# Performance work log

Hardware: AMD Instinct MI355X
Metric: run time of the kernel (lower is better)

The kernel has to match this reference:

```python
import jax, jax.numpy as jnp
import numpy as np

N, E, D, L, RBF = 20000, 320000, 128, 3, 64
CUTOFF = 5.0
LN_EPS = 1e-5


def setup_inputs() -> dict:
    key = jax.random.key(0)
    ks = jax.random.split(key, 20)
    s = 0.05
    inp = {
        'z': jax.random.normal(ks[0], (N, 64), jnp.float32),
        'pos': jax.random.normal(ks[1], (N, 3), jnp.float32),
        'edge_index': jax.random.randint(ks[2], (2, E), 0, N),
        'in_w': jax.random.normal(ks[3], (64, D), jnp.float32) * s,
        'in_b': jnp.zeros((D,), jnp.float32),
        'filt_w': jax.random.normal(ks[4], (RBF, 3 * D), jnp.float32) * s,
        'filt_b': jnp.zeros((3 * D,), jnp.float32),
        'inter_w1': jax.random.normal(ks[5], (L, D, D), jnp.float32) * s,
        'inter_b1': jnp.zeros((L, D), jnp.float32),
        'inter_w2': jax.random.normal(ks[6], (L, D, 3 * D), jnp.float32) * s,
        'inter_b2': jnp.zeros((L, 3 * D), jnp.float32),
        'mix_mu_w': jax.random.normal(ks[7], (L, D, 2 * D), jnp.float32) * s,
        'mix_w1': jax.random.normal(ks[8], (L, 2 * D, D), jnp.float32) * s,
        'mix_b1': jnp.zeros((L, D), jnp.float32),
        'mix_w2': jax.random.normal(ks[9], (L, D, 3 * D), jnp.float32) * s,
        'mix_b2': jnp.zeros((L, 3 * D), jnp.float32),
        'mu_proj_w': jnp.zeros((D,), jnp.float32),  # nn.init.constant_(0.0) in source
        'ln_g': jnp.ones((D,), jnp.float32),
        'ln_b': jnp.zeros((D,), jnp.float32),
    }
    return inp


def painn_forward(z, pos, in_w, in_b, filt_w, filt_b, inter_w1, inter_b1,
                  inter_w2, inter_b2, mix_mu_w, mix_w1, mix_b1, mix_w2, mix_b2,
                  mu_proj_w, ln_g, ln_b, edge_index):
    idx_i, idx_j = edge_index[0], edge_index[1]
    # edge geometry
    r_ij = pos[idx_j] - pos[idx_i]                               # [E,3]
    d_ij = jnp.maximum(jnp.linalg.norm(r_ij, axis=1, keepdims=True), 1e-8)  # [E,1]
    dir_ij = r_ij / d_ij                                          # [E,3]
    # gaussian smearing
    offset = jnp.linspace(0.0, CUTOFF, RBF).astype(jnp.float32)
    coeff = -0.5 / (offset[1] - offset[0]) ** 2
    phi = jnp.exp(coeff * (d_ij - offset) ** 2)                   # [E,RBF]
    # cosine cutoff
    xc = jnp.clip(d_ij / CUTOFF, 0.0, 1.0)
    fcut = 0.5 * (jnp.cos(jnp.pi * xc) + 1.0) * (xc < 1.0)        # [E,1]
    filters = (phi @ filt_w + filt_b) * fcut                      # [E,3D]
    filters = jnp.clip(jnp.nan_to_num(filters), -5.0, 5.0)
    Wij = filters[:, None, :]                                     # [E,1,3D]

    q = jax.nn.silu(z @ in_w + in_b)[:, None, :]                  # [N,1,D]
    mu = jnp.zeros((N, 3, D), q.dtype)                            # [N,3,D]

    for l in range(L):
        # interaction (edge gather -> gate -> scatter-add)
        x = jax.nn.silu(q @ inter_w1[l] + inter_b1[l]) @ inter_w2[l] + inter_b2[l]  # [N,1,3D]
        xj = x[idx_j] * Wij                                       # [E,1,3D]
        dq, dmuR, dmumu = jnp.split(xj, 3, axis=-1)               # each [E,1,D]
        muj = mu[idx_j]                                           # [E,3,D]
        q = q + jax.ops.segment_sum(dq, idx_i, num_segments=N)
        dmu = dmuR * dir_ij[:, :, None] + dmumu * muj             # [E,3,D]
        mu = mu + jax.ops.segment_sum(dmu, idx_i, num_segments=N)
        # intra-atomic mixing
        mu_mix = mu @ mix_mu_w[l]                                  # [N,3,2D]
        mu_V, mu_W = jnp.split(mu_mix, 2, axis=-1)                 # [N,3,D]
        mu_Vn = jnp.sqrt(jnp.sum(mu_V ** 2, axis=-2, keepdims=True) + 1e-8)  # [N,1,D]
        ctx = jnp.concatenate([q, mu_Vn], axis=-1)                 # [N,1,2D]
        xm = jax.nn.silu(ctx @ mix_w1[l] + mix_b1[l]) @ mix_w2[l] + mix_b2[l]  # [N,1,3D]
        dq_i, dmu_i, dqmu_i = jnp.split(xm, 3, axis=-1)
        q = q + dq_i + dqmu_i * jnp.sum(mu_V * mu_W, axis=1, keepdims=True)
        mu = mu + dmu_i * mu_W

    node_attr = jnp.clip(jnp.nan_to_num(q[:, 0, :]), -5.0, 5.0)   # [N,D]
    mean = jnp.mean(node_attr, axis=-1, keepdims=True)
    var = jnp.var(node_attr, axis=-1, keepdims=True)
    node_attr = (node_attr - mean) * jax.lax.rsqrt(var + LN_EPS) * ln_g + ln_b
    node_attr = jnp.nan_to_num(jnp.tanh(node_attr))

    mu = jnp.nan_to_num(mu)
    mu_node = jax.ops.segment_sum(mu[idx_j], idx_i, num_segments=N)  # [N,3,D]
    mu_node = jnp.clip(jnp.nan_to_num(mu_node), -5.0, 5.0)
    pos_attr = jnp.clip(jnp.nan_to_num(mu_node @ mu_proj_w), -5.0, 5.0)  # [N,3]
    return node_attr, pos_attr


def reference(z, pos, edge_index, in_w, in_b, filt_w, filt_b, inter_w1, inter_b1,
              inter_w2, inter_b2, mix_mu_w, mix_w1, mix_b1, mix_w2, mix_b2,
              mu_proj_w, ln_g, ln_b):
    return painn_forward(z, pos, in_w, in_b, filt_w, filt_b, inter_w1, inter_b1,
                         inter_w2, inter_b2, mix_mu_w, mix_w1, mix_b1, mix_w2,
                         mix_b2, mu_proj_w, ln_g, ln_b, edge_index)
```

## Files before the change

### kernel.cpp

```cpp
#include <hip/hip_runtime.h>
#include <math.h>

#ifndef M_PI
#define M_PI 3.14159265358979323846
#endif

static constexpr int N_NODES = 20000;
static constexpr int N_EDGES = 320000;
static constexpr int NLAYER  = 3;
static constexpr int NB_SCAN = (N_NODES + 255) / 256;
static constexpr int TAB_T   = 1024;

typedef _Float16 f16;
typedef __attribute__((ext_vector_type(2))) _Float16 f16x2;
typedef __attribute__((ext_vector_type(8))) _Float16 f16x8;
typedef __attribute__((ext_vector_type(4))) float f32x4;

__device__ __forceinline__ void storev(float* p, float v) { *p = v; }
__device__ __forceinline__ void storev(f16* p, float v)   { *p = (f16)v; }

__global__ void k_hist(const int* __restrict__ idx_i, int* __restrict__ cnt) {
  int e = blockIdx.x * 256 + threadIdx.x;
  if (e < N_EDGES) atomicAdd(&cnt[idx_i[e]], 1);
}

__global__ void k_scan_blk(const int* __restrict__ cnt, int* __restrict__ incl,
                           int* __restrict__ bsum) {
  __shared__ int buf[256];
  int t = threadIdx.x;
  int i = blockIdx.x * 256 + t;
  int v = (i < N_NODES) ? cnt[i] : 0;
  buf[t] = v;
  __syncthreads();
  #pragma unroll
  for (int off = 1; off < 256; off <<= 1) {
    int x = (t >= off) ? buf[t - off] : 0;
    __syncthreads();
    buf[t] += x;
    __syncthreads();
  }
  if (i < N_NODES) incl[i] = buf[t];
  if (t == 255) bsum[blockIdx.x] = buf[255];
}

__global__ void k_scan_top(int* __restrict__ bsum) {
  __shared__ int buf[128];
  int t = threadIdx.x;
  int v = (t < NB_SCAN) ? bsum[t] : 0;
  buf[t] = v;
  __syncthreads();
  #pragma unroll
  for (int off = 1; off < 128; off <<= 1) {
    int x = (t >= off) ? buf[t - off] : 0;
    __syncthreads();
    buf[t] += x;
    __syncthreads();
  }
  if (t <= NB_SCAN) bsum[t] = buf[t] - v;
}

__global__ void k_scan_add(const int* __restrict__ cnt, const int* __restrict__ incl,
                           const int* __restrict__ bsum, int* __restrict__ rs) {
  int i = blockIdx.x * 256 + threadIdx.x;
  if (i < N_NODES) rs[i] = bsum[blockIdx.x] + incl[i] - cnt[i];
  if (i == 0) rs[N_NODES] = bsum[NB_SCAN];
}

__global__ void k_fill(const int* __restrict__ idx_i, int* __restrict__ cur, int* __restrict__ eidx) {
  int e = blockIdx.x * 256 + threadIdx.x;
  if (e < N_EDGES) {
    int p = atomicAdd(&cur[idx_i[e]], 1);
    eidx[p] = e;
  }
}

__global__ void k_edge_geom(const float* __restrict__ pos, const int* __restrict__ idx_all,
                            const int* __restrict__ eidx, float4* __restrict__ geo,
                            int* __restrict__ jperm) {
  int p = blockIdx.x * 256 + threadIdx.x;
  if (p >= N_EDGES) return;
  int e = eidx[p];
  int i = idx_all[e];
  int j = idx_all[N_EDGES + e];
  float rx = pos[j*3+0] - pos[i*3+0];
  float ry = pos[j*3+1] - pos[i*3+1];
  float rz = pos[j*3+2] - pos[i*3+2];
  float d = sqrtf(rx*rx + ry*ry + rz*rz);
  d = fmaxf(d, 1e-8f);
  float inv = 1.0f / d;
  geo[p] = make_float4(d, rx*inv, ry*inv, rz*inv);
  jperm[p] = j;
}

struct WJob { const float* src; f16* dst; int kshift; int ld; int col0; int nk; };
struct WJobs { WJob j[17]; };

__global__ void k_wt_all(WJobs jb) {
  WJob w = jb.j[blockIdx.y];
  int t = blockIdx.x * 256 + threadIdx.x;
  if (t >= w.nk) return;
  int K = 1 << w.kshift;
  int n = t >> w.kshift;
  int k = t & (K - 1);
  w.dst[t] = (f16)w.src[(size_t)k * w.ld + w.col0 + n];
}

__global__ __launch_bounds__(128) void k_tab(const f16* __restrict__ wt_f ,
                                             const float* __restrict__ bias,
                                             f16* __restrict__ tab) {
  __shared__ float ph[64];
  const int t = blockIdx.x;
  const float dist = 5.0f * (float)t / (float)(TAB_T - 1);
  const int tid = threadIdx.x;
  const float delta = 5.0f / 63.0f;
  const float coeff = -0.5f / (delta * delta);
  if (tid < 64) {
    float u = dist - delta * (float)tid;
    ph[tid] = expf(coeff * u * u);
  }
  __syncthreads();
  float xc = dist * 0.2f;
  float fc = (xc < 1.0f) ? 0.5f * (cosf((float)M_PI * xc) + 1.0f) : 0.0f;
  #pragma unroll
  for (int s = 0; s < 3; ++s) {
    int n = tid + s * 128;
    const f16* wr = wt_f + (size_t)n * 64;
    float acc = 0.f;
    #pragma unroll
    for (int k = 0; k < 64; ++k) acc += ph[k] * (float)wr[k];
    float v = (acc + bias[n]) * fc;
    v = fminf(fmaxf(v, -5.0f), 5.0f);
    tab[(size_t)t * 384 + n] = (f16)v;
  }
}

template<int EPI, typename AT, typename CT>
__global__ __launch_bounds__(256) void k_mgemm(
    const AT* __restrict__ A, const f16* __restrict__ Wt,
    const float* __restrict__ bias, CT* __restrict__ C,
    int M, int K, int ldc) {
  __shared__ f16 As[128 * 32];
  __shared__ f16 Bs[128 * 32];
  const int bm = blockIdx.x * 128;
  const int bn = blockIdx.y * 128;
  const int tid = threadIdx.x;
  const int wave = tid >> 6, lane = tid & 63;
  const int wm = (wave & 1) * 64, wn = (wave >> 1) * 64;
  const int lr = lane & 15;
  const int lk = lane >> 4;
  const int srow = tid >> 1;
  const int sc0 = (tid & 1) * 2;
  const int sw = (srow >> 1) & 3;
  f32x4 acc[4][4] = {};
  for (int k0 = 0; k0 < K; k0 += 32) {
    {
      int gm = bm + srow;
      f16x8 c0, c1;
      if (gm < M) {
        if constexpr (sizeof(AT) == 2) {
          const f16* ap = (const f16*)A + (size_t)gm * K + k0 + sc0 * 8;
          c0 = *(const f16x8*)ap;
          c1 = *(const f16x8*)(ap + 8);
        } else {
          const float* ap = (const float*)A + (size_t)gm * K + k0 + sc0 * 8;
          float4 v0 = ((const float4*)ap)[0];
          float4 v1 = ((const float4*)ap)[1];
          float4 v2 = ((const float4*)ap)[2];
          float4 v3 = ((const float4*)ap)[3];
          c0[0]=(f16)v0.x; c0[1]=(f16)v0.y; c0[2]=(f16)v0.z; c0[3]=(f16)v0.w;
          c0[4]=(f16)v1.x; c0[5]=(f16)v1.y; c0[6]=(f16)v1.z; c0[7]=(f16)v1.w;
          c1[0]=(f16)v2.x; c1[1]=(f16)v2.y; c1[2]=(f16)v2.z; c1[3]=(f16)v2.w;
          c1[4]=(f16)v3.x; c1[5]=(f16)v3.y; c1[6]=(f16)v3.z; c1[7]=(f16)v3.w;
        }
      } else {
        #pragma unroll
        for (int u = 0; u < 8; ++u) { c0[u] = (f16)0.f; c1[u] = (f16)0.f; }
      }
      *(f16x8*)&As[srow * 32 + ((sc0 ^ sw) << 3)]       = c0;
      *(f16x8*)&As[srow * 32 + (((sc0 + 1) ^ sw) << 3)] = c1;
    }
    {
      const f16* bp = Wt + (size_t)(bn + srow) * K + k0 + sc0 * 8;
      f16x8 b0 = *(const f16x8*)bp;
      f16x8 b1 = *(const f16x8*)(bp + 8);
      *(f16x8*)&Bs[srow * 32 + ((sc0 ^ sw) << 3)]       = b0;
      *(f16x8*)&Bs[srow * 32 + (((sc0 + 1) ^ sw) << 3)] = b1;
    }
    __syncthreads();
    f16x8 af[4], bf[4];
    #pragma unroll
    for (int mt = 0; mt < 4; ++mt) {
      int r = wm + mt * 16 + lr;
      af[mt] = *(const f16x8*)&As[r * 32 + ((lk ^ ((r >> 1) & 3)) << 3)];
    }
    #pragma unroll
    for (int nt = 0; nt < 4; ++nt) {
      int r = wn + nt * 16 + lr;
      bf[nt] = *(const f16x8*)&Bs[r * 32 + ((lk ^ ((r >> 1) & 3)) << 3)];
    }
    #pragma unroll
    for (int mt = 0; mt < 4; ++mt)
      #pragma unroll
      for (int nt = 0; nt < 4; ++nt)
        acc[mt][nt] = __builtin_amdgcn_mfma_f32_16x16x32_f16(af[mt], bf[nt], acc[mt][nt], 0, 0, 0);
    __syncthreads();
  }
  #pragma unroll
  for (int mt = 0; mt < 4; ++mt) {
    int gm0 = bm + wm + mt * 16 + lk * 4;
    #pragma unroll
    for (int nt = 0; nt < 4; ++nt) {
      int gn = bn + wn + nt * 16 + lr;
      float bv = bias ? bias[gn] : 0.0f;
      #pragma unroll
      for (int rr = 0; rr < 4; ++rr) {
        int gm = gm0 + rr;
        if (gm >= M) continue;
        float v = acc[mt][nt][rr] + bv;
        if (EPI == 1) v = v / (1.0f + expf(-v));
        storev(&C[(size_t)gm * ldc + gn], v);
      }
    }
  }
}

__global__ __launch_bounds__(256) void k_fused_i(
    const float* __restrict__ q, const f16* __restrict__ W1, const float* __restrict__ b1,
    const f16* __restrict__ W2, const float* __restrict__ b2,
    f16* __restrict__ xout, int M) {
  __shared__ f16 As[64 * 32];
  __shared__ f16 Hs[64 * 132];
  const int tid = threadIdx.x;
  const int wave = tid >> 6, lane = tid & 63;
  const int wm = (wave & 1) * 32, wn = (wave >> 1) * 64;
  const int lr = lane & 15, lk = lane >> 4;
  const int srow = tid >> 2, c8 = tid & 3;
  const int sw = (srow >> 1) & 3;
  const int bm = blockIdx.x * 64;
  f32x4 acc[2][4] = {};
  for (int k0 = 0; k0 < 128; k0 += 32) {
    {
      int gm = bm + srow;
      f16x8 c0;
      if (gm < M) {
        const float* ap = q + (size_t)gm * 128 + k0 + c8 * 8;
        float4 v0 = ((const float4*)ap)[0];
        float4 v1 = ((const float4*)ap)[1];
        c0[0]=(f16)v0.x; c0[1]=(f16)v0.y; c0[2]=(f16)v0.z; c0[3]=(f16)v0.w;
        c0[4]=(f16)v1.x; c0[5]=(f16)v1.y; c0[6]=(f16)v1.z; c0[7]=(f16)v1.w;
      } else {
        #pragma unroll
        for (int u = 0; u < 8; ++u) c0[u] = (f16)0.f;
      }
      *(f16x8*)&As[srow * 32 + ((c8 ^ sw) << 3)] = c0;
    }
    __syncthreads();
    f16x8 af[2], bf[4];
    #pragma unroll
    for (int mt = 0; mt < 2; ++mt) {
      int r = wm + mt * 16 + lr;
      af[mt] = *(const f16x8*)&As[r * 32 + ((lk ^ ((r >> 1) & 3)) << 3)];
    }
    #pragma unroll
    for (int nt = 0; nt < 4; ++nt)
      bf[nt] = *(const f16x8*)&W1[(size_t)(wn + nt * 16 + lr) * 128 + k0 + lk * 8];
    #pragma unroll
    for (int mt = 0; mt < 2; ++mt)
      #pragma unroll
      for (int nt = 0; nt < 4; ++nt)
        acc[mt][nt] = __builtin_amdgcn_mfma_f32_16x16x32_f16(af[mt], bf[nt], acc[mt][nt], 0, 0, 0);
    __syncthreads();
  }
  #pragma unroll
  for (int mt = 0; mt < 2; ++mt)
    #pragma unroll
    for (int nt = 0; nt < 4; ++nt) {
      int col = wn + nt * 16 + lr;
      float bv = b1[col];
      #pragma unroll
      for (int rr = 0; rr < 4; ++rr) {
        int row = wm + mt * 16 + lk * 4 + rr;
        float v = acc[mt][nt][rr] + bv;
        v = v / (1.0f + expf(-v));
        Hs[row * 132 + col] = (f16)v;
      }
    }
  __syncthreads();
  #pragma unroll
  for (int cc = 0; cc < 3; ++cc) {
    f32x4 a2[2][4] = {};
    for (int k0 = 0; k0 < 128; k0 += 32) {
      f16x8 af2[2], bf2[4];
      #pragma unroll
      for (int mt = 0; mt < 2; ++mt)
        af2[mt] = *(const f16x8*)&Hs[(wm + mt * 16 + lr) * 132 + k0 + lk * 8];
      #pragma unroll
      for (int nt = 0; nt < 4; ++nt)
        bf2[nt] = *(const f16x8*)&W2[(size_t)(cc * 128 + wn + nt * 16 + lr) * 128 + k0 + lk * 8];
      #pragma unroll
      for (int mt = 0; mt < 2; ++mt)
        #pragma unroll
        for (int nt = 0; nt < 4; ++nt)
          a2[mt][nt] = __builtin_amdgcn_mfma_f32_16x16x32_f16(af2[mt], bf2[nt], a2[mt][nt], 0, 0, 0);
    }
    #pragma unroll
    for (int mt = 0; mt < 2; ++mt)
      #pragma unroll
      for (int nt = 0; nt < 4; ++nt) {
        int gn = cc * 128 + wn + nt * 16 + lr;
        float bv = b2[gn];
        #pragma unroll
        for (int rr = 0; rr < 4; ++rr) {
          int gm = bm + wm + mt * 16 + lk * 4 + rr;
          if (gm >= M) continue;
          xout[(size_t)gm * 384 + gn] = (f16)(a2[mt][nt][rr] + bv);
        }
      }
  }
}

__global__ __launch_bounds__(256) void k_fused_x(
    float* __restrict__ q,
    const f16* __restrict__ W1, const float* __restrict__ b1,
    const f16* __restrict__ W2, const float* __restrict__ b2,
    const f16* __restrict__ mumix, f16* __restrict__ mu, int M) {
  __shared__ f16 As[64 * 32];
  __shared__ f16 Hs[64 * 132];
  const int tid = threadIdx.x;
  const int wave = tid >> 6, lane = tid & 63;
  const int wm = (wave & 1) * 32, wn = (wave >> 1) * 64;
  const int lr = lane & 15, lk = lane >> 4;
  const int srow = tid >> 2, c8 = tid & 3;
  const int sw = (srow >> 1) & 3;
  const int bm = blockIdx.x * 64;
  f32x4 acc[2][4] = {};
  for (int k0 = 0; k0 < 256; k0 += 32) {
    {
      int gm = bm + srow;
      int col = k0 + c8 * 8;
      f16x8 c0;
      if (gm >= M) {
        #pragma unroll
        for (int u = 0; u < 8; ++u) c0[u] = (f16)0.f;
      } else if (col < 128) {
        const float* src = q + (size_t)gm * 128 + col;
        float4 v0 = ((const float4*)src)[0];
        float4 v1 = ((const float4*)src)[1];
        c0[0]=(f16)v0.x; c0[1]=(f16)v0.y; c0[2]=(f16)v0.z; c0[3]=(f16)v0.w;
        c0[4]=(f16)v1.x; c0[5]=(f16)v1.y; c0[6]=(f16)v1.z; c0[7]=(f16)v1.w;
      } else {
        const f16* mm = mumix + (size_t)gm * 768 + (col - 128);
        f16x8 V0 = *(const f16x8*)(mm);
        f16x8 V1 = *(const f16x8*)(mm + 256);
        f16x8 V2 = *(const f16x8*)(mm + 512);
        #pragma unroll
        for (int u = 0; u < 8; ++u) {
          float a = (float)V0[u], b_ = (float)V1[u], c = (float)V2[u];
          c0[u] = (f16)sqrtf(a*a + b_*b_ + c*c + 1e-8f);
        }
      }
      *(f16x8*)&As[srow * 32 + ((c8 ^ sw) << 3)] = c0;
    }
    __syncthreads();
    f16x8 af[2], bf[4];
    #pragma unroll
    for (int mt = 0; mt < 2; ++mt) {
      int r = wm + mt * 16 + lr;
      af[mt] = *(const f16x8*)&As[r * 32 + ((lk ^ ((r >> 1) & 3)) << 3)];
    }
    #pragma unroll
    for (int nt = 0; nt < 4; ++nt)
      bf[nt] = *(const f16x8*)&W1[(size_t)(wn + nt * 16 + lr) * 256 + k0 + lk * 8];
    #pragma unroll
    for (int mt = 0; mt < 2; ++mt)
      #pragma unroll
      for (int nt = 0; nt < 4; ++nt)
        acc[mt][nt] = __builtin_amdgcn_mfma_f32_16x16x32_f16(af[mt], bf[nt], acc[mt][nt], 0, 0, 0);
    __syncthreads();
  }
  #pragma unroll
  for (int mt = 0; mt < 2; ++mt)
    #pragma unroll
    for (int nt = 0; nt < 4; ++nt) {
      int col = wn + nt * 16 + lr;
      float bv = b1[col];
      #pragma unroll
      for (int rr = 0; rr < 4; ++rr) {
        int row = wm + mt * 16 + lk * 4 + rr;
        float v = acc[mt][nt][rr] + bv;
        v = v / (1.0f + expf(-v));
        Hs[row * 132 + col] = (f16)v;
      }
    }
  __syncthreads();
  f32x4 a2[3][2][4] = {};
  #pragma unroll
  for (int cc = 0; cc < 3; ++cc)
    for (int k0 = 0; k0 < 128; k0 += 32) {
      f16x8 af2[2], bf2[4];
      #pragma unroll
      for (int mt = 0; mt < 2; ++mt)
        af2[mt] = *(const f16x8*)&Hs[(wm + mt * 16 + lr) * 132 + k0 + lk * 8];
      #pragma unroll
      for (int nt = 0; nt < 4; ++nt)
        bf2[nt] = *(const f16x8*)&W2[(size_t)(cc * 128 + wn + nt * 16 + lr) * 128 + k0 + lk * 8];
      #pragma unroll
      for (int mt = 0; mt < 2; ++mt)
        #pragma unroll
        for (int nt = 0; nt < 4; ++nt)
          a2[cc][mt][nt] = __builtin_amdgcn_mfma_f32_16x16x32_f16(af2[mt], bf2[nt], a2[cc][mt][nt], 0, 0, 0);
    }
  #pragma unroll
  for (int mt = 0; mt < 2; ++mt)
    #pragma unroll
    for (int nt = 0; nt < 4; ++nt) {
      int col = wn + nt * 16 + lr;
      float b_dq = b2[col], b_dmu = b2[128 + col], b_dqmu = b2[256 + col];
      #pragma unroll
      for (int rr = 0; rr < 4; ++rr) {
        int gm = bm + wm + mt * 16 + lk * 4 + rr;
        if (gm >= M) continue;
        float dq   = a2[0][mt][nt][rr] + b_dq;
        float dmu  = a2[1][mt][nt][rr] + b_dmu;
        float dqmu = a2[2][mt][nt][rr] + b_dqmu;
        const f16* mm = mumix + (size_t)gm * 768;
        float V0 = (float)mm[col],       W0 = (float)mm[128 + col];
        float V1 = (float)mm[256 + col], W1v = (float)mm[384 + col];
        float V2 = (float)mm[512 + col], W2v = (float)mm[640 + col];
        float svw = V0 * W0 + V1 * W1v + V2 * W2v;
        size_t qi = (size_t)gm * 128 + col;
        q[qi] += dq + dqmu * svw;
        f16* mr = mu + (size_t)gm * 384;
        mr[col]       = (f16)((float)mr[col]       + dmu * W0);
        mr[128 + col] = (f16)((float)mr[128 + col] + dmu * W1v);
        mr[256 + col] = (f16)((float)mr[256 + col] + dmu * W2v);
      }
    }
}

__global__ __launch_bounds__(256) void k_edge_msg(
    const int* __restrict__ rs, const int* __restrict__ jperm,
    const f16* __restrict__ x, const f16* __restrict__ tab,
    const float4* __restrict__ geo, const f16* __restrict__ mu_in,
    float* __restrict__ q, f16* __restrict__ mu_out) {
  const int wid  = threadIdx.x >> 6;
  const int lane = threadIdx.x & 63;
  const int i = blockIdx.x * 4 + wid;
  if (i >= N_NODES) return;
  const int d0 = lane * 2;
  const float scale = (float)(TAB_T - 1) / 5.0f;
  float aqx = 0.f, aqy = 0.f;
  float a0x = 0.f, a0y = 0.f, a1x = 0.f, a1y = 0.f, a2x = 0.f, a2y = 0.f;
  const int s = rs[i], e = rs[i + 1];

  auto body = [&](float dx, float dy, float dz,
                  f16x2 ta0, f16x2 ta1, f16x2 ta2, f16x2 tb0, f16x2 tb1, f16x2 tb2,
                  f16x2 xv0, f16x2 xv1, f16x2 xv2, f16x2 mv0, f16x2 mv1, f16x2 mv2,
                  float fr) {
    float fo = 1.0f - fr;
    float W0x = fo * (float)ta0[0] + fr * (float)tb0[0];
    float W0y = fo * (float)ta0[1] + fr * (float)tb0[1];
    float W1x = fo * (float)ta1[0] + fr * (float)tb1[0];
    float W1y = fo * (float)ta1[1] + fr * (float)tb1[1];
    float W2x = fo * (float)ta2[0] + fr * (float)tb2[0];
    float W2y = fo * (float)ta2[1] + fr * (float)tb2[1];
    float m1x = (float)xv1[0] * W1x, m1y = (float)xv1[1] * W1y;
    float m2x = (float)xv2[0] * W2x, m2y = (float)xv2[1] * W2y;
    aqx = fmaf((float)xv0[0], W0x, aqx);
    aqy = fmaf((float)xv0[1], W0y, aqy);
    a0x += m1x * dx + m2x * (float)mv0[0];
    a0y += m1y * dx + m2y * (float)mv0[1];
    a1x += m1x * dy + m2x * (float)mv1[0];
    a1y += m1y * dy + m2y * (float)mv1[1];
    a2x += m1x * dz + m2x * (float)mv2[0];
    a2y += m1y * dz + m2y * (float)mv2[1];
  };

  int p = s;
  for (; p + 2 <= e; p += 2) {
    int jA = jperm[p], jB = jperm[p + 1];
    float4 gA = geo[p], gB = geo[p + 1];
    float uA = fminf(gA.x, 5.0f) * scale;
    float uB = fminf(gB.x, 5.0f) * scale;
    int tA = min((int)uA, TAB_T - 2);
    int tB = min((int)uB, TAB_T - 2);
    float frA = uA - (float)tA, frB = uB - (float)tB;
    const f16* taA = tab + (size_t)tA * 384;
    const f16* taB = tab + (size_t)tB * 384;
    const f16* xjA = x + (size_t)jA * 384;
    const f16* xjB = x + (size_t)jB * 384;
    const f16* mjA = mu_in + (size_t)jA * 384;
    const f16* mjB = mu_in + (size_t)jB * 384;
    f16x2 tA0 = *(const f16x2*)(taA + d0);
    f16x2 tA1 = *(const f16x2*)(taA + 128 + d0);
    f16x2 tA2 = *(const f16x2*)(taA + 256 + d0);
    f16x2 tA3 = *(const f16x2*)(taA + 384 + d0);
    f16x2 tA4 = *(const f16x2*)(taA + 512 + d0);
    f16x2 tA5 = *(const f16x2*)(taA + 640 + d0);
    f16x2 xA0 = *(const f16x2*)(xjA + d0);
    f16x2 xA1 = *(const f16x2*)(xjA + 128 + d0);
    f16x2 xA2 = *(const f16x2*)(xjA + 256 + d0);
    f16x2 mA0 = *(const f16x2*)(mjA + d0);
    f16x2 mA1 = *(const f16x2*)(mjA + 128 + d0);
    f16x2 mA2 = *(const f16x2*)(mjA + 256 + d0);
    f16x2 tB0 = *(const f16x2*)(taB + d0);
    f16x2 tB1 = *(const f16x2*)(taB + 128 + d0);
    f16x2 tB2 = *(const f16x2*)(taB + 256 + d0);
    f16x2 tB3 = *(const f16x2*)(taB + 384 + d0);
    f16x2 tB4 = *(const f16x2*)(taB + 512 + d0);
    f16x2 tB5 = *(const f16x2*)(taB + 640 + d0);
    f16x2 xB0 = *(const f16x2*)(xjB + d0);
    f16x2 xB1 = *(const f16x2*)(xjB + 128 + d0);
    f16x2 xB2 = *(const f16x2*)(xjB + 256 + d0);
    f16x2 mB0 = *(const f16x2*)(mjB + d0);
    f16x2 mB1 = *(const f16x2*)(mjB + 128 + d0);
    f16x2 mB2 = *(const f16x2*)(mjB + 256 + d0);
    body(gA.y, gA.z, gA.w, tA0, tA1, tA2, tA3, tA4, tA5,
         xA0, xA1, xA2, mA0, mA1, mA2, frA);
    body(gB.y, gB.z, gB.w, tB0, tB1, tB2, tB3, tB4, tB5,
         xB0, xB1, xB2, mB0, mB1, mB2, frB);
  }
  for (; p < e; ++p) {
    int j = jperm[p];
    float4 g = geo[p];
    float u = fminf(g.x, 5.0f) * scale;
    int t0 = min((int)u, TAB_T - 2);
    float fr = u - (float)t0;
    const f16* ta = tab + (size_t)t0 * 384;
    const f16* xj = x + (size_t)j * 384;
    const f16* mj = mu_in + (size_t)j * 384;
    body(g.y, g.z, g.w,
         *(const f16x2*)(ta + d0), *(const f16x2*)(ta + 128 + d0), *(const f16x2*)(ta + 256 + d0),
         *(const f16x2*)(ta + 384 + d0), *(const f16x2*)(ta + 512 + d0), *(const f16x2*)(ta + 640 + d0),
         *(const f16x2*)(xj + d0), *(const f16x2*)(xj + 128 + d0), *(const f16x2*)(xj + 256 + d0),
         *(const f16x2*)(mj + d0), *(const f16x2*)(mj + 128 + d0), *(const f16x2*)(mj + 256 + d0),
         fr);
  }

  float* qp = q + (size_t)i * 128 + d0;
  float2 qv = *(float2*)qp;
  qv.x += aqx; qv.y += aqy;
  *(float2*)qp = qv;
  const f16* min_ = mu_in + (size_t)i * 384;
  f16* mout = mu_out + (size_t)i * 384;
  f16x2 o0, o1, o2;
  f16x2 i0 = *(const f16x2*)(min_ + d0);
  f16x2 i1 = *(const f16x2*)(min_ + 128 + d0);
  f16x2 i2 = *(const f16x2*)(min_ + 256 + d0);
  o0[0] = (f16)((float)i0[0] + a0x); o0[1] = (f16)((float)i0[1] + a0y);
  o1[0] = (f16)((float)i1[0] + a1x); o1[1] = (f16)((float)i1[1] + a1y);
  o2[0] = (f16)((float)i2[0] + a2x); o2[1] = (f16)((float)i2[1] + a2y);
  *(f16x2*)(mout + d0)       = o0;
  *(f16x2*)(mout + 128 + d0) = o1;
  *(f16x2*)(mout + 256 + d0) = o2;
}

__global__ __launch_bounds__(256) void k_posattr(
    const int* __restrict__ rs, const int* __restrict__ jperm,
    const f16* __restrict__ mu, const float* __restrict__ w, float* __restrict__ pos_out) {
  const int wid  = threadIdx.x >> 6;
  const int lane = threadIdx.x & 63;
  const int i = blockIdx.x * 4 + wid;
  if (i >= N_NODES) return;
  const int d0 = lane * 2;
  float a0x = 0.f, a0y = 0.f, a1x = 0.f, a1y = 0.f, a2x = 0.f, a2y = 0.f;
  const int s = rs[i], e = rs[i + 1];
  int p = s;
  for (; p + 2 <= e; p += 2) {
    int jA = jperm[p], jB = jperm[p + 1];
    const f16* mA = mu + (size_t)jA * 384;
    const f16* mB = mu + (size_t)jB * 384;
    f16x2 A0 = *(const f16x2*)(mA + d0);
    f16x2 A1 = *(const f16x2*)(mA + 128 + d0);
    f16x2 A2 = *(const f16x2*)(mA + 256 + d0);
    f16x2 B0 = *(const f16x2*)(mB + d0);
    f16x2 B1 = *(const f16x2*)(mB + 128 + d0);
    f16x2 B2 = *(const f16x2*)(mB + 256 + d0);
    a0x += (float)A0[0] + (float)B0[0]; a0y += (float)A0[1] + (float)B0[1];
    a1x += (float)A1[0] + (float)B1[0]; a1y += (float)A1[1] + (float)B1[1];
    a2x += (float)A2[0] + (float)B2[0]; a2y += (float)A2[1] + (float)B2[1];
  }
  for (; p < e; ++p) {
    int j = jperm[p];
    const f16* mj = mu + (size_t)j * 384;
    f16x2 A0 = *(const f16x2*)(mj + d0);
    f16x2 A1 = *(const f16x2*)(mj + 128 + d0);
    f16x2 A2 = *(const f16x2*)(mj + 256 + d0);
    a0x += (float)A0[0]; a0y += (float)A0[1];
    a1x += (float)A1[0]; a1y += (float)A1[1];
    a2x += (float)A2[0]; a2y += (float)A2[1];
  }
  float wx = w[d0], wy = w[d0 + 1];
  float s0 = fminf(fmaxf(a0x, -5.f), 5.f) * wx + fminf(fmaxf(a0y, -5.f), 5.f) * wy;
  float s1 = fminf(fmaxf(a1x, -5.f), 5.f) * wx + fminf(fmaxf(a1y, -5.f), 5.f) * wy;
  float s2 = fminf(fmaxf(a2x, -5.f), 5.f) * wx + fminf(fmaxf(a2y, -5.f), 5.f) * wy;
  #pragma unroll
  for (int off = 32; off > 0; off >>= 1) {
    s0 += __shfl_down(s0, off, 64);
    s1 += __shfl_down(s1, off, 64);
    s2 += __shfl_down(s2, off, 64);
  }
  if (lane == 0) {
    pos_out[(size_t)i * 3 + 0] = fminf(fmaxf(s0, -5.f), 5.f);
    pos_out[(size_t)i * 3 + 1] = fminf(fmaxf(s1, -5.f), 5.f);
    pos_out[(size_t)i * 3 + 2] = fminf(fmaxf(s2, -5.f), 5.f);
  }
}

__global__ __launch_bounds__(256) void k_ln(const float* __restrict__ q, const float* __restrict__ g,
                                            const float* __restrict__ b, float* __restrict__ out) {
  const int wid = threadIdx.x >> 6, lane = threadIdx.x & 63;
  const int n = blockIdx.x * 4 + wid;
  if (n >= N_NODES) return;
  const int d0 = lane * 2;
  float2 v = *(const float2*)(q + (size_t)n * 128 + d0);
  float v0 = fminf(fmaxf(v.x, -5.f), 5.f);
  float v1 = fminf(fmaxf(v.y, -5.f), 5.f);
  float s = v0 + v1, s2 = v0 * v0 + v1 * v1;
  #pragma unroll
  for (int off = 32; off > 0; off >>= 1) {
    s  += __shfl_down(s,  off, 64);
    s2 += __shfl_down(s2, off, 64);
  }
  s  = __shfl(s,  0, 64);
  s2 = __shfl(s2, 0, 64);
  float mean = s * (1.0f / 128.0f);
  float var  = s2 * (1.0f / 128.0f) - mean * mean;
  float r = rsqrtf(var + 1e-5f);
  out[(size_t)n * 128 + d0]     = tanhf((v0 - mean) * r * g[d0]     + b[d0]);
  out[(size_t)n * 128 + d0 + 1] = tanhf((v1 - mean) * r * g[d0 + 1] + b[d0 + 1]);
}

extern "C" void kernel_launch(void* const* d_in, const int* in_sizes, int n_in,
                              void* d_out, int out_size, void* d_ws, size_t ws_size,
                              hipStream_t stream) {
  const float* z         = (const float*)d_in[0];
  const float* pos       = (const float*)d_in[1];
  const int*   edge_idx  = (const int*)d_in[2];
  const float* in_w      = (const float*)d_in[3];
  const float* in_b      = (const float*)d_in[4];
  const float* filt_w    = (const float*)d_in[5];
  const float* filt_b    = (const float*)d_in[6];
  const float* inter_w1  = (const float*)d_in[7];
  const float* inter_b1  = (const float*)d_in[8];
  const float* inter_w2  = (const float*)d_in[9];
  const float* inter_b2  = (const float*)d_in[10];
  const float* mix_mu_w  = (const float*)d_in[11];
  const float* mix_w1    = (const float*)d_in[12];
  const float* mix_b1    = (const float*)d_in[13];
  const float* mix_w2    = (const float*)d_in[14];
  const float* mix_b2    = (const float*)d_in[15];
  const float* mu_proj_w = (const float*)d_in[16];
  const float* ln_g      = (const float*)d_in[17];
  const float* ln_b      = (const float*)d_in[18];

  char* base = (char*)d_ws;
  size_t off = 0;
  auto alloc = [&](size_t bytes) -> char* {
    char* p = base + off;
    off += (bytes + 255) & ~(size_t)255;
    return p;
  };
  float*  q     = (float*)alloc((size_t)N_NODES * 128 * 4);
  f16*    x16   = (f16*)alloc((size_t)N_NODES * 384 * 2);
  f16*    mu_a  = (f16*)alloc((size_t)N_NODES * 384 * 2);
  f16*    mu_b  = (f16*)alloc((size_t)N_NODES * 384 * 2);
  f16*    mumix = (f16*)alloc((size_t)N_NODES * 768 * 2);
  float4* geo   = (float4*)alloc((size_t)N_EDGES * 16);
  int*    cnt   = (int*)alloc((size_t)N_NODES * 4);
  int*    incl  = (int*)alloc((size_t)N_NODES * 4);
  int*    bsum  = (int*)alloc(128 * 4);
  int*    rs    = (int*)alloc((size_t)(N_NODES + 1) * 4);
  int*    cur   = (int*)alloc((size_t)N_NODES * 4);
  int*    eidx  = (int*)alloc((size_t)N_EDGES * 4);
  int*    jperm = (int*)alloc((size_t)N_EDGES * 4);
  f16*    tab   = (f16*)alloc((size_t)TAB_T * 384 * 2);
  f16* wt_in = (f16*)alloc((size_t)128 * 64 * 2);
  f16* wt_f  = (f16*)alloc((size_t)384 * 64 * 2);
  f16* wt_i1 = (f16*)alloc((size_t)3 * 128 * 128 * 2);
  f16* wt_i2 = (f16*)alloc((size_t)3 * 384 * 128 * 2);
  f16* wt_mu = (f16*)alloc((size_t)3 * 256 * 128 * 2);
  f16* wt_x1 = (f16*)alloc((size_t)3 * 128 * 256 * 2);
  f16* wt_x2 = (f16*)alloc((size_t)3 * 384 * 128 * 2);
  if (off > ws_size) return;

  float* out_node = (float*)d_out;
  float* out_pos  = (float*)d_out + (size_t)N_NODES * 128;

  {
    WJobs jb;
    int ji = 0;
    jb.j[ji++] = {in_w,   wt_in, 6, 128, 0, 128 * 64};
    jb.j[ji++] = {filt_w, wt_f,  6, 384, 0, 384 * 64};
    for (int l = 0; l < 3; ++l)
      jb.j[ji++] = {inter_w1 + (size_t)l*128*128, wt_i1 + (size_t)l*128*128, 7, 128, 0, 128*128};
    for (int l = 0; l < 3; ++l)
      jb.j[ji++] = {inter_w2 + (size_t)l*128*384, wt_i2 + (size_t)l*384*128, 7, 384, 0, 384*128};
    for (int l = 0; l < 3; ++l)
      jb.j[ji++] = {mix_mu_w + (size_t)l*128*256, wt_mu + (size_t)l*256*128, 7, 256, 0, 256*128};
    for (int l = 0; l < 3; ++l)
      jb.j[ji++] = {mix_w1 + (size_t)l*256*128, wt_x1 + (size_t)l*128*256, 8, 128, 0, 128*256};
    for (int l = 0; l < 3; ++l)
      jb.j[ji++] = {mix_w2 + (size_t)l*128*384, wt_x2 + (size_t)l*384*128, 7, 384, 0, 384*128};
    dim3 g(192, 17);
    k_wt_all<<<g, 256, 0, stream>>>(jb);
  }

  k_tab<<<TAB_T, 128, 0, stream>>>(wt_f, filt_b, tab);

  hipMemsetAsync(cnt, 0, (size_t)N_NODES * 4, stream);
  k_hist<<<N_EDGES / 256, 256, 0, stream>>>(edge_idx, cnt);
  k_scan_blk<<<NB_SCAN, 256, 0, stream>>>(cnt, incl, bsum);
  k_scan_top<<<1, 128, 0, stream>>>(bsum);
  k_scan_add<<<NB_SCAN, 256, 0, stream>>>(cnt, incl, bsum, rs);
  hipMemcpyAsync(cur, rs, (size_t)N_NODES * 4, hipMemcpyDeviceToDevice, stream);
  k_fill<<<N_EDGES / 256, 256, 0, stream>>>(edge_idx, cur, eidx);

  k_edge_geom<<<N_EDGES / 256, 256, 0, stream>>>(pos, edge_idx, eidx, geo, jperm);

  dim3 ge((N_NODES + 127) / 128, 1);
  dim3 gv((N_NODES * 3 + 127) / 128, 2);
  k_mgemm<1, float, float><<<ge, 256, 0, stream>>>(z, wt_in, in_b, q, N_NODES, 64, 128);
  hipMemsetAsync(mu_a, 0, (size_t)N_NODES * 384 * 2, stream);

  f16* mu_cur = mu_a;
  f16* mu_nxt = mu_b;
  const int gn4 = (N_NODES + 3) / 4;
  const int gf  = (N_NODES + 63) / 64;
  for (int l = 0; l < NLAYER; ++l) {
    k_fused_i<<<gf, 256, 0, stream>>>(q, wt_i1 + (size_t)l*128*128, inter_b1 + (size_t)l*128,
                                      wt_i2 + (size_t)l*384*128, inter_b2 + (size_t)l*384,
                                      x16, N_NODES);
    k_edge_msg<<<gn4, 256, 0, stream>>>(rs, jperm, x16, tab, geo, mu_cur, q, mu_nxt);
    { f16* t = mu_cur; mu_cur = mu_nxt; mu_nxt = t; }
    k_mgemm<0, f16, f16><<<gv, 256, 0, stream>>>(mu_cur, wt_mu + (size_t)l*256*128, nullptr,
                                                 mumix, N_NODES * 3, 128, 256);
    k_fused_x<<<gf, 256, 0, stream>>>(q,
                                      wt_x1 + (size_t)l*128*256, mix_b1 + (size_t)l*128,
                                      wt_x2 + (size_t)l*384*128, mix_b2 + (size_t)l*384,
                                      mumix, mu_cur, N_NODES);
  }

  k_posattr<<<gn4, 256, 0, stream>>>(rs, jperm, mu_cur, mu_proj_w, out_pos);
  k_ln<<<gn4, 256, 0, stream>>>(q, ln_g, ln_b, out_node);
}
```

Before: 663.4 us.

## Fuse mu mixing GEMM into mix kernel, keeping mumix in shared memory

Merges the per-layer mu-mixing GEMM (mu @ mix_mu_w) into the mix update kernel. Each block of 32 nodes computes its 96x256 mumix tile into shared memory, then the vector norms and both MLP stages run from LDS. This removes the global write and reread of the N x 768 mumix buffer and one launch per layer. It also folds the device-to-device copy of row starts into the scan-add kernel. The cost is about 74KB of shared memory per block, which limits occupancy, and smaller 32-row tiles for the mix GEMMs.

```diff
diff --git a/kernel.cpp b/kernel.cpp
--- a/kernel.cpp
+++ b/kernel.cpp
@@ -60,9 +60,14 @@
 }
 
 __global__ void k_scan_add(const int* __restrict__ cnt, const int* __restrict__ incl,
-                           const int* __restrict__ bsum, int* __restrict__ rs) {
+                           const int* __restrict__ bsum, int* __restrict__ rs,
+                           int* __restrict__ cur) {
   int i = blockIdx.x * 256 + threadIdx.x;
-  if (i < N_NODES) rs[i] = bsum[blockIdx.x] + incl[i] - cnt[i];
+  if (i < N_NODES) {
+    int v = bsum[blockIdx.x] + incl[i] - cnt[i];
+    rs[i] = v;
+    cur[i] = v;
+  }
   if (i == 0) rs[N_NODES] = bsum[NB_SCAN];
 }
 
@@ -319,123 +324,157 @@
   }
 }
 
-__global__ __launch_bounds__(256) void k_fused_x(
-    float* __restrict__ q,
+__global__ __launch_bounds__(256) void k_fused_mx(
+    float* __restrict__ q, f16* __restrict__ mu,
+    const f16* __restrict__ Wmu,
     const f16* __restrict__ W1, const float* __restrict__ b1,
-    const f16* __restrict__ W2, const float* __restrict__ b2,
-    const f16* __restrict__ mumix, f16* __restrict__ mu, int M) {
-  __shared__ f16 As[64 * 32];
-  __shared__ f16 Hs[64 * 132];
+    const f16* __restrict__ W2, const float* __restrict__ b2) {
+  __shared__ __align__(16) char pool[50688 + 24576];
+  f16* MM  = (f16*)pool;
+  f16* As4 = (f16*)(pool + 50688);
+  f16* VN  = (f16*)(pool + 50688);
+  f16* HS  = (f16*)(pool + 50688 + 8192);
+
   const int tid = threadIdx.x;
   const int wave = tid >> 6, lane = tid & 63;
-  const int wm = (wave & 1) * 32, wn = (wave >> 1) * 64;
   const int lr = lane & 15, lk = lane >> 4;
-  const int srow = tid >> 2, c8 = tid & 3;
-  const int sw = (srow >> 1) & 3;
-  const int bm = blockIdx.x * 64;
-  f32x4 acc[2][4] = {};
-  for (int k0 = 0; k0 < 256; k0 += 32) {
-    {
-      int gm = bm + srow;
-      int col = k0 + c8 * 8;
-      f16x8 c0;
-      if (gm >= M) {
+  const int n0 = blockIdx.x * 32;
+  const int r0 = n0 * 3;
+
+  #pragma unroll
+  for (int rep = 0; rep < 6; ++rep) {
+    int idx = rep * 256 + tid;
+    int row = idx >> 4;
+    int g   = idx & 15;
+    int kb = g >> 2, c8 = g & 3;
+    f16x8 v = *(const f16x8*)(mu + (size_t)(r0 + row) * 128 + g * 8);
+    *(f16x8*)&As4[((kb * 96 + row) << 5) + (((c8 ^ ((row >> 1) & 3))) << 3)] = v;
+  }
+  __syncthreads();
+
+  const int wmA = (wave & 1) * 48;
+  const int wnA0 = (wave >> 1) * 64;
+  #pragma unroll
+  for (int half = 0; half < 2; ++half) {
+    f32x4 accA[3][4] = {};
+    #pragma unroll
+    for (int kk = 0; kk < 4; ++kk) {
+      f16x8 af[3], bf[4];
+      #pragma unroll
+      for (int mt = 0; mt < 3; ++mt) {
+        int r = wmA + mt * 16 + lr;
+        af[mt] = *(const f16x8*)&As4[((kk * 96 + r) << 5) + ((lk ^ ((r >> 1) & 3)) << 3)];
+      }
+      #pragma unroll
+      for (int nt = 0; nt < 4; ++nt)
+        bf[nt] = *(const f16x8*)&Wmu[(size_t)(half * 128 + wnA0 + nt * 16 + lr) * 128 + kk * 32 + lk * 8];
+      #pragma unroll
+      for (int mt = 0; mt < 3; ++mt)
         #pragma unroll
-        for (int u = 0; u < 8; ++u) c0[u] = (f16)0.f;
-      } else if (col < 128) {
-        const float* src = q + (size_t)gm * 128 + col;
-        float4 v0 = ((const float4*)src)[0];
-        float4 v1 = ((const float4*)src)[1];
-        c0[0]=(f16)v0.x; c0[1]=(f16)v0.y; c0[2]=(f16)v0.z; c0[3]=(f16)v0.w;
-        c0[4]=(f16)v1.x; c0[5]=(f16)v1.y; c0[6]=(f16)v1.z; c0[7]=(f16)v1.w;
-      } else {
-        const f16* mm = mumix + (size_t)gm * 768 + (col - 128);
-        f16x8 V0 = *(const f16x8*)(mm);
-        f16x8 V1 = *(const f16x8*)(mm + 256);
-        f16x8 V2 = *(const f16x8*)(mm + 512);
+        for (int nt = 0; nt < 4; ++nt)
+          accA[mt][nt] = __builtin_amdgcn_mfma_f32_16x16x32_f16(af[mt], bf[nt], accA[mt][nt], 0, 0, 0);
+    }
+    #pragma unroll
+    for (int mt = 0; mt < 3; ++mt)
+      #pragma unroll
+      for (int nt = 0; nt < 4; ++nt) {
+        int col = half * 128 + wnA0 + nt * 16 + lr;
         #pragma unroll
-        for (int u = 0; u < 8; ++u) {
-          float a = (float)V0[u], b_ = (float)V1[u], c = (float)V2[u];
-          c0[u] = (f16)sqrtf(a*a + b_*b_ + c*c + 1e-8f);
+        for (int rr = 0; rr < 4; ++rr) {
+          int row = wmA + mt * 16 + lk * 4 + rr;
+          MM[row * 264 + col] = (f16)accA[mt][nt][rr];
         }
       }
-      *(f16x8*)&As[srow * 32 + ((c8 ^ sw) << 3)] = c0;
-    }
-    __syncthreads();
-    f16x8 af[2], bf[4];
-    #pragma unroll
-    for (int mt = 0; mt < 2; ++mt) {
-      int r = wm + mt * 16 + lr;
-      af[mt] = *(const f16x8*)&As[r * 32 + ((lk ^ ((r >> 1) & 3)) << 3)];
-    }
+  }
+  __syncthreads();
+
+  #pragma unroll
+  for (int rep = 0; rep < 16; ++rep) {
+    int idx = rep * 256 + tid;
+    int nn = idx >> 7, c = idx & 127;
+    float V0 = (float)MM[(nn * 3 + 0) * 264 + c];
+    float V1 = (float)MM[(nn * 3 + 1) * 264 + c];
+    float V2 = (float)MM[(nn * 3 + 2) * 264 + c];
+    float vnv = sqrtf(V0 * V0 + V1 * V1 + V2 * V2 + 1e-8f);
+    int kb = c >> 5, c8 = (c >> 3) & 3, ce = c & 7;
+    VN[((kb * 32 + nn) << 5) + ((c8 ^ ((nn >> 1) & 3)) << 3) + ce] = (f16)vnv;
+  }
+  __syncthreads();
+
+  const int wmB = (wave & 1) * 16, wnB = (wave >> 1) * 64;
+  f32x4 accB[4] = {};
+  #pragma unroll
+  for (int kk = 0; kk < 8; ++kk) {
+    f16x8 af;
+    int row = wmB + lr;
+    if (kk < 4) {
+      const float* qp_ = q + (size_t)(n0 + row) * 128 + kk * 32 + lk * 8;
+      float4 v0 = ((const float4*)qp_)[0];
+      float4 v1 = ((const float4*)qp_)[1];
+      af[0]=(f16)v0.x; af[1]=(f16)v0.y; af[2]=(f16)v0.z; af[3]=(f16)v0.w;
+      af[4]=(f16)v1.x; af[5]=(f16)v1.y; af[6]=(f16)v1.z; af[7]=(f16)v1.w;
+    } else {
+      af = *(const f16x8*)&VN[(((kk - 4) * 32 + row) << 5) + ((lk ^ ((row >> 1) & 3)) << 3)];
+    }
+    f16x8 bf[4];
     #pragma unroll
     for (int nt = 0; nt < 4; ++nt)
-      bf[nt] = *(const f16x8*)&W1[(size_t)(wn + nt * 16 + lr) * 256 + k0 + lk * 8];
-    #pragma unroll
-    for (int mt = 0; mt < 2; ++mt)
+      bf[nt] = *(const f16x8*)&W1[(size_t)(wnB + nt * 16 + lr) * 256 + kk * 32 + lk * 8];
+    #pragma unroll
+    for (int nt = 0; nt < 4; ++nt)
+      accB[nt] = __builtin_amdgcn_mfma_f32_16x16x32_f16(af, bf[nt], accB[nt], 0, 0, 0);
+  }
+  #pragma unroll
+  for (int nt = 0; nt < 4; ++nt) {
+    int col = wnB + nt * 16 + lr;
+    float bv = b1[col];
+    #pragma unroll
+    for (int rr = 0; rr < 4; ++rr) {
+      int row = wmB + lk * 4 + rr;
+      float v = accB[nt][rr] + bv;
+      v = v / (1.0f + expf(-v));
+      HS[row * 132 + col] = (f16)v;
+    }
+  }
+  __syncthreads();
+
+  f32x4 accC[3][4] = {};
+  #pragma unroll
+  for (int cc = 0; cc < 3; ++cc)
+    #pragma unroll
+    for (int kk = 0; kk < 4; ++kk) {
+      f16x8 af = *(const f16x8*)&HS[(wmB + lr) * 132 + kk * 32 + lk * 8];
+      f16x8 bf[4];
       #pragma unroll
       for (int nt = 0; nt < 4; ++nt)
-        acc[mt][nt] = __builtin_amdgcn_mfma_f32_16x16x32_f16(af[mt], bf[nt], acc[mt][nt], 0, 0, 0);
-    __syncthreads();
-  }
-  #pragma unroll
-  for (int mt = 0; mt < 2; ++mt)
-    #pragma unroll
-    for (int nt = 0; nt < 4; ++nt) {
-      int col = wn + nt * 16 + lr;
-      float bv = b1[col];
-      #pragma unroll
-      for (int rr = 0; rr < 4; ++rr) {
-        int row = wm + mt * 16 + lk * 4 + rr;
-        float v = acc[mt][nt][rr] + bv;
-        v = v / (1.0f + expf(-v));
-        Hs[row * 132 + col] = (f16)v;
-      }
-    }
-  __syncthreads();
-  f32x4 a2[3][2][4] = {};
-  #pragma unroll
-  for (int cc = 0; cc < 3; ++cc)
-    for (int k0 = 0; k0 < 128; k0 += 32) {
-      f16x8 af2[2], bf2[4];
-      #pragma unroll
-      for (int mt = 0; mt < 2; ++mt)
-        af2[mt] = *(const f16x8*)&Hs[(wm + mt * 16 + lr) * 132 + k0 + lk * 8];
+        bf[nt] = *(const f16x8*)&W2[(size_t)(cc * 128 + wnB + nt * 16 + lr) * 128 + kk * 32 + lk * 8];
       #pragma unroll
       for (int nt = 0; nt < 4; ++nt)
-        bf2[nt] = *(const f16x8*)&W2[(size_t)(cc * 128 + wn + nt * 16 + lr) * 128 + k0 + lk * 8];
-      #pragma unroll
-      for (int mt = 0; mt < 2; ++mt)
-        #pragma unroll
-        for (int nt = 0; nt < 4; ++nt)
-          a2[cc][mt][nt] = __builtin_amdgcn_mfma_f32_16x16x32_f16(af2[mt], bf2[nt], a2[cc][mt][nt], 0, 0, 0);
-    }
-  #pragma unroll
-  for (int mt = 0; mt < 2; ++mt)
-    #pragma unroll
-    for (int nt = 0; nt < 4; ++nt) {
-      int col = wn + nt * 16 + lr;
-      float b_dq = b2[col], b_dmu = b2[128 + col], b_dqmu = b2[256 + col];
-      #pragma unroll
-      for (int rr = 0; rr < 4; ++rr) {
-        int gm = bm + wm + mt * 16 + lk * 4 + rr;
-        if (gm >= M) continue;
-        float dq   = a2[0][mt][nt][rr] + b_dq;
-        float dmu  = a2[1][mt][nt][rr] + b_dmu;
-        float dqmu = a2[2][mt][nt][rr] + b_dqmu;
-        const f16* mm = mumix + (size_t)gm * 768;
-        float V0 = (float)mm[col],       W0 = (float)mm[128 + col];
-        float V1 = (float)mm[256 + col], W1v = (float)mm[384 + col];
-        float V2 = (float)mm[512 + col], W2v = (float)mm[640 + col];
-        float svw = V0 * W0 + V1 * W1v + V2 * W2v;
-        size_t qi = (size_t)gm * 128 + col;
-        q[qi] += dq + dqmu * svw;
-        f16* mr = mu + (size_t)gm * 384;
-        mr[col]       = (f16)((float)mr[col]       + dmu * W0);
-        mr[128 + col] = (f16)((float)mr[128 + col] + dmu * W1v);
-        mr[256 + col] = (f16)((float)mr[256 + col] + dmu * W2v);
-      }
-    }
+        accC[cc][nt] = __builtin_amdgcn_mfma_f32_16x16x32_f16(af, bf[nt], accC[cc][nt], 0, 0, 0);
+    }
+  #pragma unroll
+  for (int nt = 0; nt < 4; ++nt) {
+    int col = wnB + nt * 16 + lr;
+    float b_dq = b2[col], b_dmu = b2[128 + col], b_dqmu = b2[256 + col];
+    #pragma unroll
+    for (int rr = 0; rr < 4; ++rr) {
+      int nn = wmB + lk * 4 + rr;
+      int gm = n0 + nn;
+      float dq   = accC[0][nt][rr] + b_dq;
+      float dmu  = accC[1][nt][rr] + b_dmu;
+      float dqmu = accC[2][nt][rr] + b_dqmu;
+      float V0 = (float)MM[(nn * 3 + 0) * 264 + col], W0 = (float)MM[(nn * 3 + 0) * 264 + 128 + col];
+      float V1 = (float)MM[(nn * 3 + 1) * 264 + col], W1v = (float)MM[(nn * 3 + 1) * 264 + 128 + col];
+      float V2 = (float)MM[(nn * 3 + 2) * 264 + col], W2v = (float)MM[(nn * 3 + 2) * 264 + 128 + col];
+      float svw = V0 * W0 + V1 * W1v + V2 * W2v;
+      size_t qi = (size_t)gm * 128 + col;
+      q[qi] += dq + dqmu * svw;
+      f16* mr = mu + (size_t)gm * 384;
+      mr[col]       = (f16)((float)mr[col]       + dmu * W0);
+      mr[128 + col] = (f16)((float)mr[128 + col] + dmu * W1v);
+      mr[256 + col] = (f16)((float)mr[256 + col] + dmu * W2v);
+    }
+  }
 }
 
 __global__ __launch_bounds__(256) void k_edge_msg(
@@ -665,7 +704,6 @@
   f16*    x16   = (f16*)alloc((size_t)N_NODES * 384 * 2);
   f16*    mu_a  = (f16*)alloc((size_t)N_NODES * 384 * 2);
   f16*    mu_b  = (f16*)alloc((size_t)N_NODES * 384 * 2);
-  f16*    mumix = (f16*)alloc((size_t)N_NODES * 768 * 2);
   float4* geo   = (float4*)alloc((size_t)N_EDGES * 16);
   int*    cnt   = (int*)alloc((size_t)N_NODES * 4);
   int*    incl  = (int*)alloc((size_t)N_NODES * 4);
@@ -712,14 +750,12 @@
   k_hist<<<N_EDGES / 256, 256, 0, stream>>>(edge_idx, cnt);
   k_scan_blk<<<NB_SCAN, 256, 0, stream>>>(cnt, incl, bsum);
   k_scan_top<<<1, 128, 0, stream>>>(bsum);
-  k_scan_add<<<NB_SCAN, 256, 0, stream>>>(cnt, incl, bsum, rs);
-  hipMemcpyAsync(cur, rs, (size_t)N_NODES * 4, hipMemcpyDeviceToDevice, stream);
+  k_scan_add<<<NB_SCAN, 256, 0, stream>>>(cnt, incl, bsum, rs, cur);
   k_fill<<<N_EDGES / 256, 256, 0, stream>>>(edge_idx, cur, eidx);
 
   k_edge_geom<<<N_EDGES / 256, 256, 0, stream>>>(pos, edge_idx, eidx, geo, jperm);
 
   dim3 ge((N_NODES + 127) / 128, 1);
-  dim3 gv((N_NODES * 3 + 127) / 128, 2);
   k_mgemm<1, float, float><<<ge, 256, 0, stream>>>(z, wt_in, in_b, q, N_NODES, 64, 128);
   hipMemsetAsync(mu_a, 0, (size_t)N_NODES * 384 * 2, stream);
 
@@ -727,18 +763,16 @@
   f16* mu_nxt = mu_b;
   const int gn4 = (N_NODES + 3) / 4;
   const int gf  = (N_NODES + 63) / 64;
+  const int gmx = N_NODES / 32;
   for (int l = 0; l < NLAYER; ++l) {
     k_fused_i<<<gf, 256, 0, stream>>>(q, wt_i1 + (size_t)l*128*128, inter_b1 + (size_t)l*128,
                                       wt_i2 + (size_t)l*384*128, inter_b2 + (size_t)l*384,
                                       x16, N_NODES);
     k_edge_msg<<<gn4, 256, 0, stream>>>(rs, jperm, x16, tab, geo, mu_cur, q, mu_nxt);
     { f16* t = mu_cur; mu_cur = mu_nxt; mu_nxt = t; }
-    k_mgemm<0, f16, f16><<<gv, 256, 0, stream>>>(mu_cur, wt_mu + (size_t)l*256*128, nullptr,
-                                                 mumix, N_NODES * 3, 128, 256);
-    k_fused_x<<<gf, 256, 0, stream>>>(q,
-                                      wt_x1 + (size_t)l*128*256, mix_b1 + (size_t)l*128,
-                                      wt_x2 + (size_t)l*384*128, mix_b2 + (size_t)l*384,
-                                      mumix, mu_cur, N_NODES);
+    k_fused_mx<<<gmx, 256, 0, stream>>>(q, mu_cur, wt_mu + (size_t)l*256*128,
+                                        wt_x1 + (size_t)l*128*256, mix_b1 + (size_t)l*128,
+                                        wt_x2 + (size_t)l*384*128, mix_b2 + (size_t)l*384);
   }
 
   k_posattr<<<gn4, 256, 0, stream>>>(rs, jperm, mu_cur, mu_proj_w, out_pos);
```

After: 613.5 us. 1.08x faster.
